# Kernel tuning notes

Hardware: AMD Instinct MI355X
Metric: run time of the kernel (lower is better)

The kernel has to match this reference:

```python
import jax, jax.numpy as jnp
import numpy as np

H = 512  # hidden_size


def setup_inputs() -> dict:
    key = jax.random.key(0)
    k1, k2, k3, k4, k5 = jax.random.split(key, 5)
    B, S = 32, 2048
    hidden = jax.random.normal(k1, (1, B, H), dtype=jnp.float32)
    encoder_outputs = jax.random.normal(k2, (B, S, 2 * H), dtype=jnp.float32)
    # nn.Linear(3H, H): weight [H, 3H], store transposed [3H, H] for x @ W
    scale_a = 1.0 / np.sqrt(3 * H)
    Wa = jax.random.uniform(k3, (3 * H, H), jnp.float32, -scale_a, scale_a)
    ba = jax.random.uniform(k4, (H,), jnp.float32, -scale_a, scale_a)
    # nn.Linear(H, 1, bias=False): weight [1, H] -> store as [H]
    scale_v = 1.0 / np.sqrt(H)
    v = jax.random.uniform(k5, (H,), jnp.float32, -scale_v, scale_v)
    return {"hidden": hidden, "encoder_outputs": encoder_outputs,
            "Wa": Wa, "ba": ba, "v": v}


def reference(hidden, encoder_outputs, Wa, ba, v):
    # hidden: [1, B, H] -> [B, H]; encoder_outputs: [B, S, 2H]
    h = jnp.squeeze(hidden, axis=0)                      # [B, H]
    # Split concat-linear into two projections (same math as cat + matmul):
    Wh, We = Wa[:H], Wa[H:]                              # [H, H], [2H, H]
    # energy: [B, S, H] = tanh(h Wh + enc We + b), h broadcast over S
    energy = jnp.tanh(h @ Wh + jnp.einsum('bse,eh->bsh', encoder_outputs, We)[..., :, :] + ba) if False else \
             jnp.tanh((h @ Wh)[:, None, :] + jnp.einsum('bse,eh->bsh', encoder_outputs, We) + ba)
    scores = jnp.einsum('bsh,h->bs', energy, v)          # [B, S]
    attention_weights = jax.nn.softmax(scores, axis=1)   # [B, S]
    context = jnp.einsum('bs,bse->be', attention_weights, encoder_outputs)  # [B, 2H]
    return context, attention_weights
```

## Files before the change

kernel.cpp:

```cpp
#include <hip/hip_runtime.h>

typedef unsigned short ushort_t;
typedef __attribute__((ext_vector_type(8))) short bf16x8;
typedef __attribute__((ext_vector_type(4))) float f32x4;

#define H 512
#define E 1024
#define S 2048
#define B 32
#define NCHUNK (S / 64)

__device__ __forceinline__ ushort_t f2bf(float f) {
    unsigned u = __float_as_uint(f);
    unsigned r = (u + 0x7FFFu + ((u >> 16) & 1u)) >> 16;
    return (ushort_t)r;
}

__device__ __forceinline__ unsigned pkbf(float x, float y) {
    unsigned u0 = __float_as_uint(x) + 0x8000u;
    unsigned u1 = __float_as_uint(y) + 0x8000u;
    return __builtin_amdgcn_perm(u1, u0, 0x07060302u);
}

__device__ __forceinline__ float fast_tanh(float x) {
    float e = __expf(2.f * x);
    return 1.f - 2.f / (e + 1.f);
}

__global__ void prep_hb(const float* __restrict__ hidden, const float* __restrict__ Wa,
                        const float* __restrict__ ba, float* __restrict__ hb) {
    int b = blockIdx.x, kc = blockIdx.y, tid = threadIdx.x;
    const float* hp = hidden + b * H + kc * 64;
    float a0 = 0.f, a1 = 0.f;
    #pragma unroll 8
    for (int k = 0; k < 64; ++k) {
        float hv = hp[k];
        a0 += hv * Wa[(size_t)(kc * 64 + k) * H + tid];
        a1 += hv * Wa[(size_t)(kc * 64 + k) * H + tid + 256];
    }
    if (kc == 0) { a0 += ba[tid]; a1 += ba[tid + 256]; }
    atomicAdd(&hb[b * H + tid], a0);
    atomicAdd(&hb[b * H + tid + 256], a1);
}

__global__ void prep_wef(const float* __restrict__ Wa, ushort_t* __restrict__ wef) {
    int g = blockIdx.x * 256 + threadIdx.x;
    int kt = g >> 11, nt = (g >> 6) & 31, l = g & 63;
    int kbase = kt * 32 + ((l >> 4) << 3);
    int n = nt * 16 + (l & 15);
    #pragma unroll
    for (int j = 0; j < 8; ++j)
        wef[(size_t)g * 8 + j] = f2bf(Wa[(size_t)(H + kbase + j) * H + n]);
}

__launch_bounds__(256, 2)
__global__ void score_kernel(const float* __restrict__ enc, const ushort_t* __restrict__ wef,
                             const float* __restrict__ hb, const float* __restrict__ v,
                             float* __restrict__ scores, float* __restrict__ mpart,
                             float* __restrict__ lpart, float* __restrict__ ctxp) {
    int sc = blockIdx.x;
    int b = blockIdx.y;
    int s0 = sc * 64;
    int tid = threadIdx.x;
    int wave = tid >> 6, lane = tid & 63;
    int q = lane >> 4, nl = lane & 15;

    __shared__ char arena[65536];
    char* wbuf = arena + wave * 16384;
    float* sred = (float*)arena;
    float* lds_p = (float*)arena + 256;

    f32x4 acc[4][8] = {};
    bf16x8 bregA[8], bregB[8];

    int r0 = lane >> 3;
    int c4 = ((lane & 7) ^ (lane >> 3)) * 4;
    const float* asrc = enc + ((size_t)b * S + s0 + r0) * E + c4;
    const bf16x8* bsrc = (const bf16x8*)wef + (size_t)(wave * 8) * 64 + lane;

#define STAGE_A(KT)                                                                      \
    {                                                                                    \
        char* al = wbuf + ((KT) & 1) * 8192;                                             \
        _Pragma("unroll")                                                                \
        for (int j = 0; j < 8; ++j)                                                      \
            __builtin_amdgcn_global_load_lds(                                            \
                (const __attribute__((address_space(1))) unsigned*)                      \
                    (asrc + (size_t)(KT) * 32 + j * 8 * E),                              \
                (__attribute__((address_space(3))) unsigned*)(al + j * 1024), 16, 0, 0); \
    }

#define LOADB(BREG, KT)                                                                  \
    _Pragma("unroll")                                                                    \
    for (int ntl = 0; ntl < 8; ++ntl) BREG[ntl] = bsrc[(size_t)(KT) * 2048 + ntl * 64];

#define COMPUTE(KT, BREG)                                                                \
    {                                                                                    \
        const float* Ac = (const float*)(wbuf + ((KT) & 1) * 8192);                      \
        bf16x8 afr[4];                                                                   \
        _Pragma("unroll")                                                                \
        for (int mt = 0; mt < 4; ++mt) {                                                 \
            int r = mt * 16 + nl;                                                        \
            int sa = r * 8 + ((2 * q) ^ (nl & 7));                                       \
            int sb = r * 8 + ((2 * q + 1) ^ (nl & 7));                                   \
            float4 f0 = *(const float4*)(Ac + sa * 4);                                   \
            float4 f1 = *(const float4*)(Ac + sb * 4);                                   \
            uint4 u;                                                                     \
            u.x = pkbf(f0.x, f0.y); u.y = pkbf(f0.z, f0.w);                              \
            u.z = pkbf(f1.x, f1.y); u.w = pkbf(f1.z, f1.w);                              \
            afr[mt] = *(bf16x8*)&u;                                                      \
        }                                                                                \
        _Pragma("unroll")                                                                \
        for (int ntl = 0; ntl < 8; ++ntl) {                                              \
            _Pragma("unroll")                                                            \
            for (int mt = 0; mt < 4; ++mt)                                               \
                acc[mt][ntl] = __builtin_amdgcn_mfma_f32_16x16x32_bf16(                  \
                    afr[mt], BREG[ntl], acc[mt][ntl], 0, 0, 0);                          \
        }                                                                                \
    }

    STAGE_A(0);
    __builtin_amdgcn_sched_barrier(0);
    LOADB(bregA, 0);
    __builtin_amdgcn_sched_barrier(0);

#define FULL_ITER(T, BCUR, BNEXT)                                                        \
    STAGE_A((T) + 1);                                                                    \
    __builtin_amdgcn_sched_barrier(0);                                                   \
    LOADB(BNEXT, (T) + 1);                                                               \
    __builtin_amdgcn_sched_barrier(0);                                                   \
    asm volatile("s_waitcnt vmcnt(24)" ::: "memory");                                    \
    __builtin_amdgcn_sched_barrier(0);                                                   \
    COMPUTE((T), BCUR);

    for (int it = 0; it < 15; ++it) {
        FULL_ITER(it * 2, bregA, bregB);
        FULL_ITER(it * 2 + 1, bregB, bregA);
    }
    FULL_ITER(30, bregA, bregB);
    asm volatile("s_waitcnt vmcnt(8)" ::: "memory");
    __builtin_amdgcn_sched_barrier(0);
    COMPUTE(31, bregB);
    __syncthreads();

    float p[16];
    #pragma unroll
    for (int i = 0; i < 16; ++i) p[i] = 0.f;
    #pragma unroll
    for (int ntl = 0; ntl < 8; ++ntl) {
        int n = wave * 128 + ntl * 16 + nl;
        float hv = hb[b * H + n];
        float vv = v[n];
        #pragma unroll
        for (int mt = 0; mt < 4; ++mt)
            #pragma unroll
            for (int r = 0; r < 4; ++r)
                p[mt * 4 + r] += vv * fast_tanh(acc[mt][ntl][r] + hv);
    }
    #pragma unroll
    for (int off = 1; off < 16; off <<= 1) {
        #pragma unroll
        for (int i = 0; i < 16; ++i) p[i] += __shfl_xor(p[i], off, 64);
    }
    if (nl == 0) {
        #pragma unroll
        for (int mt = 0; mt < 4; ++mt)
            #pragma unroll
            for (int r = 0; r < 4; ++r)
                sred[wave * 64 + mt * 16 + q * 4 + r] = p[mt * 4 + r];
    }
    __syncthreads();

    if (tid < 64) {
        float s = sred[tid] + sred[64 + tid] + sred[128 + tid] + sred[192 + tid];
        scores[(size_t)b * S + s0 + tid] = s;
        float m = s;
        #pragma unroll
        for (int off = 32; off; off >>= 1) m = fmaxf(m, __shfl_xor(m, off, 64));
        float pe = __expf(s - m);
        lds_p[tid] = pe;
        float l = pe;
        #pragma unroll
        for (int off = 32; off; off >>= 1) l += __shfl_xor(l, off, 64);
        if (tid == 0) { mpart[b * NCHUNK + sc] = m; lpart[b * NCHUNK + sc] = l; }
    }
    __syncthreads();

    const float* ep = enc + ((size_t)b * S + s0) * E + tid * 4;
    float cx = 0.f, cy = 0.f, cz = 0.f, cw = 0.f;
    #pragma unroll 8
    for (int s = 0; s < 64; ++s) {
        float ps = lds_p[s];
        float4 x = *(const float4*)(ep + (size_t)s * E);
        cx += ps * x.x; cy += ps * x.y; cz += ps * x.z; cw += ps * x.w;
    }
    float4 co = {cx, cy, cz, cw};
    *(float4*)(ctxp + ((size_t)(b * NCHUNK + sc)) * E + tid * 4) = co;
#undef STAGE_A
#undef LOADB
#undef COMPUTE
#undef FULL_ITER
}

__global__ void combine_kernel(const float* __restrict__ scores, const float* __restrict__ mpart,
                               const float* __restrict__ lpart, const float* __restrict__ ctxp,
                               float* __restrict__ out) {
    int b = blockIdx.x, tid = threadIdx.x;
    __shared__ float sscale[NCHUNK];
    __shared__ float sml[2];
    if (tid < NCHUNK) {
        float m = mpart[b * NCHUNK + tid];
        float M = m;
        #pragma unroll
        for (int off = 16; off; off >>= 1) M = fmaxf(M, __shfl_xor(M, off, 64));
        float e = __expf(m - M);
        float l = lpart[b * NCHUNK + tid] * e;
        float L = l;
        #pragma unroll
        for (int off = 16; off; off >>= 1) L += __shfl_xor(L, off, 64);
        sscale[tid] = e;
        if (tid == 0) { sml[0] = M; sml[1] = L; }
    }
    __syncthreads();
    float M = sml[0], invL = 1.0f / sml[1];
    int e0 = tid * 4;
    float cx = 0.f, cy = 0.f, cz = 0.f, cw = 0.f;
    #pragma unroll 4
    for (int i = 0; i < NCHUNK; ++i) {
        float scv = sscale[i];
        float4 x = *(const float4*)(ctxp + ((size_t)(b * NCHUNK + i)) * E + e0);
        cx += scv * x.x; cy += scv * x.y; cz += scv * x.z; cw += scv * x.w;
    }
    float4 co = {cx * invL, cy * invL, cz * invL, cw * invL};
    *(float4*)(out + (size_t)b * E + e0) = co;
    const float* srow = scores + (size_t)b * S;
    float* wrow = out + B * E + (size_t)b * S;
    #pragma unroll
    for (int j = 0; j < 8; ++j) {
        int s = tid + j * 256;
        wrow[s] = __expf(srow[s] - M) * invL;
    }
}

extern "C" void kernel_launch(void* const* d_in, const int* in_sizes, int n_in,
                              void* d_out, int out_size, void* d_ws, size_t ws_size,
                              hipStream_t stream) {
    const float* hidden = (const float*)d_in[0];
    const float* enc    = (const float*)d_in[1];
    const float* Wa     = (const float*)d_in[2];
    const float* ba     = (const float*)d_in[3];
    const float* v      = (const float*)d_in[4];
    float* out = (float*)d_out;

    char* ws = (char*)d_ws;
    ushort_t* wef = (ushort_t*)ws;
    float* hb     = (float*)(ws + (1 << 20));
    float* scores = (float*)(ws + (1 << 20) + (1 << 16));
    float* mpart  = (float*)(ws + (1 << 20) + (1 << 16) + (1 << 18));
    float* lpart  = mpart + B * NCHUNK;
    float* ctxp   = (float*)(ws + (1 << 20) + (1 << 16) + (1 << 18) + (1 << 14));

    hipMemsetAsync(hb, 0, B * H * sizeof(float), stream);
    prep_hb<<<dim3(B, 8), 256, 0, stream>>>(hidden, Wa, ba, hb);
    prep_wef<<<256, 256, 0, stream>>>(Wa, wef);
    score_kernel<<<dim3(NCHUNK, B), 256, 0, stream>>>(enc, wef, hb, v,
                                                      scores, mpart, lpart, ctxp);
    combine_kernel<<<B, 256, 0, stream>>>(scores, mpart, lpart, ctxp, out);
}
```

Measured before the change: 463.1 us.

## Halve score tile to 32 rows, single-buffer B regs, raise occupancy

Shrinks each score block from 64 to 32 sequence rows, doubling the grid to 64 chunks per batch and halving LDS and accumulator registers so three blocks fit per CU. The B-fragment register double buffer is replaced by a single buffer loaded each iteration, waited on together with the next A stage. The aim is more resident waves and better load balance across CUs. In exchange the Wa bf16 fragments are re-read twice as often per row, there is less latency hiding per wave, and the combine kernel has more partial context vectors to merge.

```diff
diff --git a/kernel.cpp b/kernel.cpp
--- a/kernel.cpp
+++ b/kernel.cpp
@@ -8,7 +8,7 @@
 #define E 1024
 #define S 2048
 #define B 32
-#define NCHUNK (S / 64)
+#define NCH 64
 
 __device__ __forceinline__ ushort_t f2bf(float f) {
     unsigned u = __float_as_uint(f);
@@ -53,25 +53,25 @@
         wef[(size_t)g * 8 + j] = f2bf(Wa[(size_t)(H + kbase + j) * H + n]);
 }
 
-__launch_bounds__(256, 2)
+__launch_bounds__(256, 3)
 __global__ void score_kernel(const float* __restrict__ enc, const ushort_t* __restrict__ wef,
                              const float* __restrict__ hb, const float* __restrict__ v,
                              float* __restrict__ scores, float* __restrict__ mpart,
                              float* __restrict__ lpart, float* __restrict__ ctxp) {
     int sc = blockIdx.x;
     int b = blockIdx.y;
-    int s0 = sc * 64;
+    int s0 = sc * 32;
     int tid = threadIdx.x;
     int wave = tid >> 6, lane = tid & 63;
     int q = lane >> 4, nl = lane & 15;
 
-    __shared__ char arena[65536];
-    char* wbuf = arena + wave * 16384;
+    __shared__ char arena[32768];
+    char* wbuf = arena + wave * 8192;
     float* sred = (float*)arena;
-    float* lds_p = (float*)arena + 256;
-
-    f32x4 acc[4][8] = {};
-    bf16x8 bregA[8], bregB[8];
+    float* lds_p = (float*)arena + 128;
+
+    f32x4 acc[2][8] = {};
+    bf16x8 breg[8];
 
     int r0 = lane >> 3;
     int c4 = ((lane & 7) ^ (lane >> 3)) * 4;
@@ -80,25 +80,25 @@
 
 #define STAGE_A(KT)                                                                      \
     {                                                                                    \
-        char* al = wbuf + ((KT) & 1) * 8192;                                             \
+        char* al = wbuf + ((KT) & 1) * 4096;                                             \
         _Pragma("unroll")                                                                \
-        for (int j = 0; j < 8; ++j)                                                      \
+        for (int j = 0; j < 4; ++j)                                                      \
             __builtin_amdgcn_global_load_lds(                                            \
                 (const __attribute__((address_space(1))) unsigned*)                      \
                     (asrc + (size_t)(KT) * 32 + j * 8 * E),                              \
                 (__attribute__((address_space(3))) unsigned*)(al + j * 1024), 16, 0, 0); \
     }
 
-#define LOADB(BREG, KT)                                                                  \
+#define LOADB(KT)                                                                        \
     _Pragma("unroll")                                                                    \
-    for (int ntl = 0; ntl < 8; ++ntl) BREG[ntl] = bsrc[(size_t)(KT) * 2048 + ntl * 64];
-
-#define COMPUTE(KT, BREG)                                                                \
+    for (int ntl = 0; ntl < 8; ++ntl) breg[ntl] = bsrc[(size_t)(KT) * 2048 + ntl * 64];
+
+#define COMPUTE(KT)                                                                      \
     {                                                                                    \
-        const float* Ac = (const float*)(wbuf + ((KT) & 1) * 8192);                      \
-        bf16x8 afr[4];                                                                   \
+        const float* Ac = (const float*)(wbuf + ((KT) & 1) * 4096);                      \
+        bf16x8 afr[2];                                                                   \
         _Pragma("unroll")                                                                \
-        for (int mt = 0; mt < 4; ++mt) {                                                 \
+        for (int mt = 0; mt < 2; ++mt) {                                                 \
             int r = mt * 16 + nl;                                                        \
             int sa = r * 8 + ((2 * q) ^ (nl & 7));                                       \
             int sb = r * 8 + ((2 * q + 1) ^ (nl & 7));                                   \
@@ -112,46 +112,41 @@
         _Pragma("unroll")                                                                \
         for (int ntl = 0; ntl < 8; ++ntl) {                                              \
             _Pragma("unroll")                                                            \
-            for (int mt = 0; mt < 4; ++mt)                                               \
+            for (int mt = 0; mt < 2; ++mt)                                               \
                 acc[mt][ntl] = __builtin_amdgcn_mfma_f32_16x16x32_bf16(                  \
-                    afr[mt], BREG[ntl], acc[mt][ntl], 0, 0, 0);                          \
+                    afr[mt], breg[ntl], acc[mt][ntl], 0, 0, 0);                          \
         }                                                                                \
     }
 
     STAGE_A(0);
     __builtin_amdgcn_sched_barrier(0);
-    LOADB(bregA, 0);
+    #pragma unroll 1
+    for (int t = 0; t < 31; ++t) {
+        LOADB(t);
+        __builtin_amdgcn_sched_barrier(0);
+        STAGE_A(t + 1);
+        __builtin_amdgcn_sched_barrier(0);
+        asm volatile("s_waitcnt vmcnt(4)" ::: "memory");
+        __builtin_amdgcn_sched_barrier(0);
+        COMPUTE(t);
+    }
+    LOADB(31);
     __builtin_amdgcn_sched_barrier(0);
-
-#define FULL_ITER(T, BCUR, BNEXT)                                                        \
-    STAGE_A((T) + 1);                                                                    \
-    __builtin_amdgcn_sched_barrier(0);                                                   \
-    LOADB(BNEXT, (T) + 1);                                                               \
-    __builtin_amdgcn_sched_barrier(0);                                                   \
-    asm volatile("s_waitcnt vmcnt(24)" ::: "memory");                                    \
-    __builtin_amdgcn_sched_barrier(0);                                                   \
-    COMPUTE((T), BCUR);
-
-    for (int it = 0; it < 15; ++it) {
-        FULL_ITER(it * 2, bregA, bregB);
-        FULL_ITER(it * 2 + 1, bregB, bregA);
-    }
-    FULL_ITER(30, bregA, bregB);
-    asm volatile("s_waitcnt vmcnt(8)" ::: "memory");
+    asm volatile("s_waitcnt vmcnt(0)" ::: "memory");
     __builtin_amdgcn_sched_barrier(0);
-    COMPUTE(31, bregB);
-    __syncthreads();
-
-    float p[16];
-    #pragma unroll
-    for (int i = 0; i < 16; ++i) p[i] = 0.f;
+    COMPUTE(31);
+    __syncthreads();
+
+    float p[8];
+    #pragma unroll
+    for (int i = 0; i < 8; ++i) p[i] = 0.f;
     #pragma unroll
     for (int ntl = 0; ntl < 8; ++ntl) {
         int n = wave * 128 + ntl * 16 + nl;
         float hv = hb[b * H + n];
         float vv = v[n];
         #pragma unroll
-        for (int mt = 0; mt < 4; ++mt)
+        for (int mt = 0; mt < 2; ++mt)
             #pragma unroll
             for (int r = 0; r < 4; ++r)
                 p[mt * 4 + r] += vv * fast_tanh(acc[mt][ntl][r] + hv);
@@ -159,64 +154,63 @@
     #pragma unroll
     for (int off = 1; off < 16; off <<= 1) {
         #pragma unroll
-        for (int i = 0; i < 16; ++i) p[i] += __shfl_xor(p[i], off, 64);
+        for (int i = 0; i < 8; ++i) p[i] += __shfl_xor(p[i], off, 64);
     }
     if (nl == 0) {
         #pragma unroll
-        for (int mt = 0; mt < 4; ++mt)
+        for (int mt = 0; mt < 2; ++mt)
             #pragma unroll
             for (int r = 0; r < 4; ++r)
-                sred[wave * 64 + mt * 16 + q * 4 + r] = p[mt * 4 + r];
-    }
-    __syncthreads();
-
-    if (tid < 64) {
-        float s = sred[tid] + sred[64 + tid] + sred[128 + tid] + sred[192 + tid];
+                sred[wave * 32 + mt * 16 + q * 4 + r] = p[mt * 4 + r];
+    }
+    __syncthreads();
+
+    if (tid < 32) {
+        float s = sred[tid] + sred[32 + tid] + sred[64 + tid] + sred[96 + tid];
         scores[(size_t)b * S + s0 + tid] = s;
         float m = s;
         #pragma unroll
-        for (int off = 32; off; off >>= 1) m = fmaxf(m, __shfl_xor(m, off, 64));
+        for (int off = 16; off; off >>= 1) m = fmaxf(m, __shfl_xor(m, off, 64));
         float pe = __expf(s - m);
         lds_p[tid] = pe;
         float l = pe;
         #pragma unroll
-        for (int off = 32; off; off >>= 1) l += __shfl_xor(l, off, 64);
-        if (tid == 0) { mpart[b * NCHUNK + sc] = m; lpart[b * NCHUNK + sc] = l; }
+        for (int off = 16; off; off >>= 1) l += __shfl_xor(l, off, 64);
+        if (tid == 0) { mpart[b * NCH + sc] = m; lpart[b * NCH + sc] = l; }
     }
     __syncthreads();
 
     const float* ep = enc + ((size_t)b * S + s0) * E + tid * 4;
     float cx = 0.f, cy = 0.f, cz = 0.f, cw = 0.f;
     #pragma unroll 8
-    for (int s = 0; s < 64; ++s) {
+    for (int s = 0; s < 32; ++s) {
         float ps = lds_p[s];
         float4 x = *(const float4*)(ep + (size_t)s * E);
         cx += ps * x.x; cy += ps * x.y; cz += ps * x.z; cw += ps * x.w;
     }
     float4 co = {cx, cy, cz, cw};
-    *(float4*)(ctxp + ((size_t)(b * NCHUNK + sc)) * E + tid * 4) = co;
+    *(float4*)(ctxp + ((size_t)(b * NCH + sc)) * E + tid * 4) = co;
 #undef STAGE_A
 #undef LOADB
 #undef COMPUTE
-#undef FULL_ITER
 }
 
 __global__ void combine_kernel(const float* __restrict__ scores, const float* __restrict__ mpart,
                                const float* __restrict__ lpart, const float* __restrict__ ctxp,
                                float* __restrict__ out) {
     int b = blockIdx.x, tid = threadIdx.x;
-    __shared__ float sscale[NCHUNK];
+    __shared__ float sscale[NCH];
     __shared__ float sml[2];
-    if (tid < NCHUNK) {
-        float m = mpart[b * NCHUNK + tid];
+    if (tid < NCH) {
+        float m = mpart[b * NCH + tid];
         float M = m;
         #pragma unroll
-        for (int off = 16; off; off >>= 1) M = fmaxf(M, __shfl_xor(M, off, 64));
+        for (int off = 32; off; off >>= 1) M = fmaxf(M, __shfl_xor(M, off, 64));
         float e = __expf(m - M);
-        float l = lpart[b * NCHUNK + tid] * e;
+        float l = lpart[b * NCH + tid] * e;
         float L = l;
         #pragma unroll
-        for (int off = 16; off; off >>= 1) L += __shfl_xor(L, off, 64);
+        for (int off = 32; off; off >>= 1) L += __shfl_xor(L, off, 64);
         sscale[tid] = e;
         if (tid == 0) { sml[0] = M; sml[1] = L; }
     }
@@ -225,9 +219,9 @@
     int e0 = tid * 4;
     float cx = 0.f, cy = 0.f, cz = 0.f, cw = 0.f;
     #pragma unroll 4
-    for (int i = 0; i < NCHUNK; ++i) {
+    for (int i = 0; i < NCH; ++i) {
         float scv = sscale[i];
-        float4 x = *(const float4*)(ctxp + ((size_t)(b * NCHUNK + i)) * E + e0);
+        float4 x = *(const float4*)(ctxp + ((size_t)(b * NCH + i)) * E + e0);
         cx += scv * x.x; cy += scv * x.y; cz += scv * x.z; cw += scv * x.w;
     }
     float4 co = {cx * invL, cy * invL, cz * invL, cw * invL};
@@ -256,13 +250,13 @@
     float* hb     = (float*)(ws + (1 << 20));
     float* scores = (float*)(ws + (1 << 20) + (1 << 16));
     float* mpart  = (float*)(ws + (1 << 20) + (1 << 16) + (1 << 18));
-    float* lpart  = mpart + B * NCHUNK;
-    float* ctxp   = (float*)(ws + (1 << 20) + (1 << 16) + (1 << 18) + (1 << 14));
+    float* lpart  = mpart + B * NCH;
+    float* ctxp   = (float*)(ws + (1 << 20) + (1 << 16) + (1 << 18) + (1 << 16));
 
     hipMemsetAsync(hb, 0, B * H * sizeof(float), stream);
     prep_hb<<<dim3(B, 8), 256, 0, stream>>>(hidden, Wa, ba, hb);
     prep_wef<<<256, 256, 0, stream>>>(Wa, wef);
-    score_kernel<<<dim3(NCHUNK, B), 256, 0, stream>>>(enc, wef, hb, v,
+    score_kernel<<<dim3(S / 32, B), 256, 0, stream>>>(enc, wef, hb, v,
                                                       scores, mpart, lpart, ctxp);
     combine_kernel<<<B, 256, 0, stream>>>(scores, mpart, lpart, ctxp, out);
 }
```

Result: slower. 508.7 us (+9.8%).

## Load encoder tiles straight into registers instead of LDS staging

Applied to the files above, without the earlier changes.

Drops the per-wave double-buffered LDS staging of encoder rows (global_load_lds plus swizzled LDS reads). Each lane now loads its MFMA A-fragment directly from global memory into registers, one k-step ahead. Weight fragments are loaded into a single register buffer each iteration rather than double-buffered. This cuts the shared-memory footprint from 64 KB to about 1 KB and removes the LDS round trip. In exchange, the weight-load latency is exposed before every MFMA batch, and the global access pattern becomes less coalesced.

```diff
diff --git a/kernel.cpp b/kernel.cpp
--- a/kernel.cpp
+++ b/kernel.cpp
@@ -65,82 +65,75 @@
     int wave = tid >> 6, lane = tid & 63;
     int q = lane >> 4, nl = lane & 15;
 
-    __shared__ char arena[65536];
-    char* wbuf = arena + wave * 16384;
-    float* sred = (float*)arena;
-    float* lds_p = (float*)arena + 256;
+    __shared__ float sred[256];
+    __shared__ float lds_p[64];
 
     f32x4 acc[4][8] = {};
-    bf16x8 bregA[8], bregB[8];
-
-    int r0 = lane >> 3;
-    int c4 = ((lane & 7) ^ (lane >> 3)) * 4;
-    const float* asrc = enc + ((size_t)b * S + s0 + r0) * E + c4;
-    const bf16x8* bsrc = (const bf16x8*)wef + (size_t)(wave * 8) * 64 + lane;
-
-#define STAGE_A(KT)                                                                      \
-    {                                                                                    \
-        char* al = wbuf + ((KT) & 1) * 8192;                                             \
+    bf16x8 breg[8];
+    bf16x8 afr[4];
+    float4 a0[4], a1[4];
+
+    const float* ap = enc + ((size_t)b * S + s0 + nl) * E + 8 * q;
+    const bf16x8* bp = (const bf16x8*)wef + (size_t)(wave * 8) * 64 + lane;
+
+#define LOADA()                                                                          \
+    _Pragma("unroll")                                                                    \
+    for (int mt = 0; mt < 4; ++mt) {                                                     \
+        a0[mt] = *(const float4*)(ap + (size_t)mt * 16 * E);                             \
+        a1[mt] = *(const float4*)(ap + (size_t)mt * 16 * E + 4);                         \
+    }
+
+#define LOADB()                                                                          \
+    _Pragma("unroll")                                                                    \
+    for (int ntl = 0; ntl < 8; ++ntl) breg[ntl] = bp[ntl * 64];
+
+#define PACK()                                                                           \
+    _Pragma("unroll")                                                                    \
+    for (int mt = 0; mt < 4; ++mt) {                                                     \
+        uint4 u;                                                                         \
+        u.x = pkbf(a0[mt].x, a0[mt].y); u.y = pkbf(a0[mt].z, a0[mt].w);                  \
+        u.z = pkbf(a1[mt].x, a1[mt].y); u.w = pkbf(a1[mt].z, a1[mt].w);                  \
+        afr[mt] = *(bf16x8*)&u;                                                          \
+    }
+
+#define MFMA_ALL()                                                                       \
+    _Pragma("unroll")                                                                    \
+    for (int ntl = 0; ntl < 8; ++ntl) {                                                  \
         _Pragma("unroll")                                                                \
-        for (int j = 0; j < 8; ++j)                                                      \
-            __builtin_amdgcn_global_load_lds(                                            \
-                (const __attribute__((address_space(1))) unsigned*)                      \
-                    (asrc + (size_t)(KT) * 32 + j * 8 * E),                              \
-                (__attribute__((address_space(3))) unsigned*)(al + j * 1024), 16, 0, 0); \
-    }
-
-#define LOADB(BREG, KT)                                                                  \
-    _Pragma("unroll")                                                                    \
-    for (int ntl = 0; ntl < 8; ++ntl) BREG[ntl] = bsrc[(size_t)(KT) * 2048 + ntl * 64];
-
-#define COMPUTE(KT, BREG)                                                                \
-    {                                                                                    \
-        const float* Ac = (const float*)(wbuf + ((KT) & 1) * 8192);                      \
-        bf16x8 afr[4];                                                                   \
-        _Pragma("unroll")                                                                \
-        for (int mt = 0; mt < 4; ++mt) {                                                 \
-            int r = mt * 16 + nl;                                                        \
-            int sa = r * 8 + ((2 * q) ^ (nl & 7));                                       \
-            int sb = r * 8 + ((2 * q + 1) ^ (nl & 7));                                   \
-            float4 f0 = *(const float4*)(Ac + sa * 4);                                   \
-            float4 f1 = *(const float4*)(Ac + sb * 4);                                   \
-            uint4 u;                                                                     \
-            u.x = pkbf(f0.x, f0.y); u.y = pkbf(f0.z, f0.w);                              \
-            u.z = pkbf(f1.x, f1.y); u.w = pkbf(f1.z, f1.w);                              \
-            afr[mt] = *(bf16x8*)&u;                                                      \
-        }                                                                                \
-        _Pragma("unroll")                                                                \
-        for (int ntl = 0; ntl < 8; ++ntl) {                                              \
-            _Pragma("unroll")                                                            \
-            for (int mt = 0; mt < 4; ++mt)                                               \
-                acc[mt][ntl] = __builtin_amdgcn_mfma_f32_16x16x32_bf16(                  \
-                    afr[mt], BREG[ntl], acc[mt][ntl], 0, 0, 0);                          \
-        }                                                                                \
-    }
-
-    STAGE_A(0);
-    __builtin_amdgcn_sched_barrier(0);
-    LOADB(bregA, 0);
-    __builtin_amdgcn_sched_barrier(0);
-
-#define FULL_ITER(T, BCUR, BNEXT)                                                        \
-    STAGE_A((T) + 1);                                                                    \
-    __builtin_amdgcn_sched_barrier(0);                                                   \
-    LOADB(BNEXT, (T) + 1);                                                               \
-    __builtin_amdgcn_sched_barrier(0);                                                   \
-    asm volatile("s_waitcnt vmcnt(24)" ::: "memory");                                    \
-    __builtin_amdgcn_sched_barrier(0);                                                   \
-    COMPUTE((T), BCUR);
-
-    for (int it = 0; it < 15; ++it) {
-        FULL_ITER(it * 2, bregA, bregB);
-        FULL_ITER(it * 2 + 1, bregB, bregA);
-    }
-    FULL_ITER(30, bregA, bregB);
+        for (int mt = 0; mt < 4; ++mt)                                                   \
+            acc[mt][ntl] = __builtin_amdgcn_mfma_f32_16x16x32_bf16(                      \
+                afr[mt], breg[ntl], acc[mt][ntl], 0, 0, 0);                              \
+    }
+
+    LOADA();
+    __builtin_amdgcn_sched_barrier(0);
+    ap += 32;
+
+    #pragma unroll 1
+    for (int t = 0; t < 31; ++t) {
+        LOADB();
+        __builtin_amdgcn_sched_barrier(0);
+        asm volatile("s_waitcnt vmcnt(8)" ::: "memory");
+        __builtin_amdgcn_sched_barrier(0);
+        PACK();
+        __builtin_amdgcn_sched_barrier(0);
+        LOADA();
+        __builtin_amdgcn_sched_barrier(0);
+        asm volatile("s_waitcnt vmcnt(8)" ::: "memory");
+        __builtin_amdgcn_sched_barrier(0);
+        MFMA_ALL();
+        ap += 32;
+        bp += 2048;
+    }
+    LOADB();
+    __builtin_amdgcn_sched_barrier(0);
     asm volatile("s_waitcnt vmcnt(8)" ::: "memory");
     __builtin_amdgcn_sched_barrier(0);
-    COMPUTE(31, bregB);
-    __syncthreads();
+    PACK();
+    __builtin_amdgcn_sched_barrier(0);
+    asm volatile("s_waitcnt vmcnt(0)" ::: "memory");
+    __builtin_amdgcn_sched_barrier(0);
+    MFMA_ALL();
 
     float p[16];
     #pragma unroll
@@ -195,10 +188,10 @@
     }
     float4 co = {cx, cy, cz, cw};
     *(float4*)(ctxp + ((size_t)(b * NCHUNK + sc)) * E + tid * 4) = co;
-#undef STAGE_A
+#undef LOADA
 #undef LOADB
-#undef COMPUTE
-#undef FULL_ITER
+#undef PACK
+#undef MFMA_ALL
 }
 
 __global__ void combine_kernel(const float* __restrict__ scores, const float* __restrict__ mpart,
```

Result: slower. 497.8 us (+7.5%).
